# Kernel tuning notes

Measured on AMD Instinct MI355X. Metric: run time of the kernel, lower is better.

## Reference

```python
import jax, jax.numpy as jnp
import numpy as np

L, I, H = 4, 256, 512          # layers, input_size, hidden_size
SH, LH, GH = 4, 2, 2            # short/long/global heads
NH, HD, FF = SH + LH + GH, H // (SH + LH + GH), 2 * H
S, B = 1024, 8                  # seq (AST nodes), batch
EPS = 1e-5
NEG = -1e9


def _ln(x, g, b):
    m = jnp.mean(x, axis=-1, keepdims=True)
    v = jnp.var(x, axis=-1, keepdims=True)
    return (x - m) * jax.lax.rsqrt(v + EPS) * g + b


def setup_inputs() -> dict:
    key = jax.random.key(0)
    ks = jax.random.split(key, 10)
    w = lambda k, shape: jax.random.normal(k, shape, jnp.float32) * 0.02
    return {
        "nodes": jax.random.normal(ks[0], (S, B, I), jnp.float32),
        "dist": jax.random.randint(ks[1], (B, S, S), 0, 5, jnp.int32),
        "dense_w": w(ks[2], (H, I)), "dense_b": jnp.zeros((H,), jnp.float32),
        "dense_ln_g": jnp.ones((H,), jnp.float32), "dense_ln_b": jnp.zeros((H,), jnp.float32),
        "qkv_w": w(ks[3], (L, 3 * H, H)), "qkv_b": jnp.zeros((L, 3 * H), jnp.float32),
        "out_w": w(ks[4], (L, H, H)), "out_b": jnp.zeros((L, H), jnp.float32),
        "ln1_g": jnp.ones((L, H), jnp.float32), "ln1_b": jnp.zeros((L, H), jnp.float32),
        "ffn_w1": w(ks[5], (L, FF, H)), "ffn_b1": jnp.zeros((L, FF), jnp.float32),
        "ffn_w2": w(ks[6], (L, H, FF)), "ffn_b2": jnp.zeros((L, H), jnp.float32),
        "ln2_g": jnp.ones((L, H), jnp.float32), "ln2_b": jnp.zeros((L, H), jnp.float32),
        "bn_g": jnp.ones((H,), jnp.float32), "bn_b": jnp.zeros((H,), jnp.float32),
    }


def _mask_bias(dist):
    # dist: [B,S,S] int -> additive bias [B,NH,S,S]
    short = (dist == 1)[:, None]                       # [B,1,S,S]
    longm = (dist >= 1)[:, None]
    globm = jnp.broadcast_to((dist[:, 0:1, :] >= 1)[:, None], (dist.shape[0], 1, S, S))
    allowed = jnp.concatenate([
        jnp.broadcast_to(short, (dist.shape[0], SH, S, S)),
        jnp.broadcast_to(longm, (dist.shape[0], LH, S, S)),
        jnp.broadcast_to(globm, (dist.shape[0], GH, S, S)),
    ], axis=1)
    allowed = allowed | jnp.eye(S, dtype=bool)
    return jnp.where(allowed, 0.0, NEG).astype(jnp.float32)


def _forward(nodes, dist, dense_w, dense_b, dense_ln_g, dense_ln_b,
             qkv_w, qkv_b, out_w, out_b, ln1_g, ln1_b,
             ffn_w1, ffn_b1, ffn_w2, ffn_b2, ln2_g, ln2_b, bn_g, bn_b):
    x = jnp.transpose(nodes, (1, 0, 2))                # [B,S,I]
    x = _ln(x @ dense_w.T + dense_b, dense_ln_g, dense_ln_b)  # [B,S,H]
    bias = _mask_bias(dist)                            # [B,NH,S,S]
    scale = 1.0 / np.sqrt(HD)

    def layer(x, p):
        (wqkv, bqkv, wo, bo, g1, b1, w1, bf1, w2, bf2, g2, b2) = p
        qkv = x @ wqkv.T + bqkv                        # [B,S,3H]
        q, k, v = jnp.split(qkv, 3, axis=-1)
        q = q.reshape(B, S, NH, HD).transpose(0, 2, 1, 3)
        k = k.reshape(B, S, NH, HD).transpose(0, 2, 1, 3)
        v = v.reshape(B, S, NH, HD).transpose(0, 2, 1, 3)
        scores = jnp.einsum('bhqd,bhkd->bhqk', q, k) * scale + bias
        attn = jax.nn.softmax(scores, axis=-1)
        o = jnp.einsum('bhqk,bhkd->bhqd', attn, v)
        o = o.transpose(0, 2, 1, 3).reshape(B, S, H) @ wo.T + bo
        x = _ln(x + o, g1, b1)
        f = jax.nn.relu(x @ w1.T + bf1) @ w2.T + bf2
        x = _ln(x + f, g2, b2)
        return x, None

    params = (qkv_w, qkv_b, out_w, out_b, ln1_g, ln1_b,
              ffn_w1, ffn_b1, ffn_w2, ffn_b2, ln2_g, ln2_b)
    x, _ = jax.lax.scan(layer, x, params)
    hidden = x[:, 0]                                   # first token -> [B,H]
    m = jnp.mean(hidden, axis=0)
    v = jnp.var(hidden, axis=0)
    return (hidden - m) * jax.lax.rsqrt(v + EPS) * bn_g + bn_b


def reference(nodes, dist, dense_w, dense_b, dense_ln_g, dense_ln_b,
              qkv_w, qkv_b, out_w, out_b, ln1_g, ln1_b,
              ffn_w1, ffn_b1, ffn_w2, ffn_b2, ln2_g, ln2_b, bn_g, bn_b):
    return _forward(nodes, dist, dense_w, dense_b, dense_ln_g, dense_ln_b,
                    qkv_w, qkv_b, out_w, out_b, ln1_g, ln1_b,
                    ffn_w1, ffn_b1, ffn_w2, ffn_b2, ln2_g, ln2_b, bn_g, bn_b)
```

## Files before the change

### kernel.cpp

```cpp
#include <hip/hip_runtime.h>
#include <hip/hip_bf16.h>
#include <math.h>

#define LAYERS 4
#define IDIM 256
#define HDIM 512
#define NH 8
#define HD 64
#define FF 1024
#define SEQ 1024
#define BATCH 8
#define EPS 1e-5f

typedef __attribute__((ext_vector_type(8))) short short8;
typedef __attribute__((ext_vector_type(4))) short short4v;
typedef __attribute__((ext_vector_type(4))) float f32x4;
typedef __attribute__((ext_vector_type(4))) int int4v;
typedef __attribute__((ext_vector_type(2))) unsigned int uint2v;
typedef unsigned long long u64;

__device__ __forceinline__ short f2bf(float f) {
    unsigned u = __float_as_uint(f);
    u = (u + 0x7FFFu + ((u >> 16) & 1u)) >> 16;
    return (short)u;
}
__device__ __forceinline__ float bf2f(short s) {
    return __uint_as_float(((unsigned)(unsigned short)s) << 16);
}
__device__ __forceinline__ void gll16(const void* g, void* l) {
    __builtin_amdgcn_global_load_lds(
        (const __attribute__((address_space(1))) unsigned int*)g,
        (__attribute__((address_space(3))) unsigned int*)l, 16, 0, 0);
}

#define CVT_P0 131072u
#define CVT_P1 3276800u
#define CVT_P2 4325376u
#define CVT_P3 6422528u
#define CVT_TOT 8519680u
__global__ __launch_bounds__(256) void cvt_all(const float* __restrict__ s0, short* __restrict__ d0,
                                               const float* __restrict__ s1, short* __restrict__ d1,
                                               const float* __restrict__ s2, short* __restrict__ d2,
                                               const float* __restrict__ s3, short* __restrict__ d3,
                                               const float* __restrict__ s4, short* __restrict__ d4) {
    size_t i = ((size_t)blockIdx.x * 256 + threadIdx.x) * 4;
    const float* s; short* d; size_t off;
    if (i < CVT_P0)      { s = s0; d = d0; off = i; }
    else if (i < CVT_P1) { s = s1; d = d1; off = i - CVT_P0; }
    else if (i < CVT_P2) { s = s2; d = d2; off = i - CVT_P1; }
    else if (i < CVT_P3) { s = s3; d = d3; off = i - CVT_P2; }
    else                 { s = s4; d = d4; off = i - CVT_P3; }
    f32x4 f = *(const f32x4*)(s + off);
    short4v o = {f2bf(f[0]), f2bf(f[1]), f2bf(f[2]), f2bf(f[3])};
    *(short4v*)(d + off) = o;
}

__global__ __launch_bounds__(256) void transpose_nodes(const float* __restrict__ nodes,
                                                       short* __restrict__ xt) {
    size_t idx = ((size_t)blockIdx.x * 256 + threadIdx.x) * 4;
    int i  = idx & (IDIM - 1);
    int sb = idx >> 8;
    int b  = sb & (BATCH - 1);
    int s  = sb >> 3;
    f32x4 f = *(const f32x4*)(nodes + idx);
    short4v o = {f2bf(f[0]), f2bf(f[1]), f2bf(f[2]), f2bf(f[3])};
    *(short4v*)(xt + ((size_t)b * SEQ + s) * IDIM + i) = o;
}

__global__ __launch_bounds__(256) void build_masks(const int* __restrict__ dist,
                                                   u64* __restrict__ mS,
                                                   u64* __restrict__ mL,
                                                   u64* __restrict__ mG) {
    int t = blockIdx.x * 256 + threadIdx.x;
    int w = t & 15, q = (t >> 4) & 1023, b = t >> 14;
    const int4v* dp = (const int4v*)(dist + ((size_t)b * SEQ + q) * SEQ + w * 64);
    u64 bs = 0, bl = 0;
#pragma unroll
    for (int i = 0; i < 16; i++) {
        int4v d = dp[i];
#pragma unroll
        for (int j = 0; j < 4; j++) {
            bs |= (u64)(d[j] == 1) << (i * 4 + j);
            bl |= (u64)(d[j] >= 1) << (i * 4 + j);
        }
    }
    mS[((size_t)b * SEQ + q) * 16 + w] = bs;
    mL[((size_t)b * SEQ + q) * 16 + w] = bl;
    if (q == 0) mG[b * 16 + w] = bl;
}

template<int BM>
__global__ __launch_bounds__(256, 2)
void gemm_bf16(const short* __restrict__ A, const short* __restrict__ W,
               const float* __restrict__ bias, short* __restrict__ C,
               short* __restrict__ vt, int M, int N, int K, int relu) {
    __shared__ __align__(16) short As[BM * 64];
    __shared__ __align__(16) short Ws[128 * 64];
    const int tid = threadIdx.x;
    const int w = tid >> 6, lane = tid & 63;
    const int l15 = lane & 15, quad = lane >> 4;
    const int m0 = blockIdx.y * BM, n0 = blockIdx.x * 128;

    constexpr int NI = (BM == 128) ? 4 : 2;
    const int wm = (BM == 128) ? (w >> 1) * 64 : 0;
    const int wn = (BM == 128) ? (w & 1) * 64 : w * 32;

    f32x4 acc[4][NI];
#pragma unroll
    for (int mi = 0; mi < 4; mi++)
#pragma unroll
        for (int ni = 0; ni < NI; ni++) acc[mi][ni] = (f32x4){0.f, 0.f, 0.f, 0.f};

    const int r_in = lane >> 3;
    const int c8   = lane & 7;

    for (int k0 = 0; k0 < K; k0 += 64) {
#pragma unroll
        for (int rep = 0; rep < BM * 8 / 256; rep++) {
            int chunk = rep * 4 + w;
            int row = chunk * 8 + r_in;
            const short* src = A + (size_t)(m0 + row) * K + k0 + ((c8 ^ (row & 7)) << 3);
            gll16(src, (char*)As + chunk * 1024);
        }
#pragma unroll
        for (int rep = 0; rep < 4; rep++) {
            int chunk = rep * 4 + w;
            int row = chunk * 8 + r_in;
            const short* src = W + (size_t)(n0 + row) * K + k0 + ((c8 ^ (row & 7)) << 3);
            gll16(src, (char*)Ws + chunk * 1024);
        }
        __syncthreads();
#pragma unroll
        for (int ks = 0; ks < 2; ks++) {
            short8 af[4], wf[NI];
            const int dblk = ks * 4 + quad;
#pragma unroll
            for (int mi = 0; mi < 4; mi++) {
                int row = wm + mi * 16 + l15;
                af[mi] = *(const short8*)((const char*)As + row * 128 + ((dblk ^ (row & 7)) << 4));
            }
#pragma unroll
            for (int ni = 0; ni < NI; ni++) {
                int row = wn + ni * 16 + l15;
                wf[ni] = *(const short8*)((const char*)Ws + row * 128 + ((dblk ^ (row & 7)) << 4));
            }
#pragma unroll
            for (int mi = 0; mi < 4; mi++)
#pragma unroll
                for (int ni = 0; ni < NI; ni++)
                    acc[mi][ni] = __builtin_amdgcn_mfma_f32_16x16x32_bf16(
                        af[mi], wf[ni], acc[mi][ni], 0, 0, 0);
        }
        __syncthreads();
    }
    if (vt && n0 >= 1024) {
#pragma unroll
        for (int ni = 0; ni < NI; ni++) {
            int n = n0 + wn + ni * 16 + l15;
            int d = n - 1024, h = d >> 6, dd = d & 63;
            float bz = bias[n];
#pragma unroll
            for (int mi = 0; mi < 4; mi++) {
                int mbase = m0 + wm + mi * 16 + quad * 4;
                int b = mbase >> 10, s = mbase & 1023;
                int tile = s >> 6, j = (s & 63) >> 2;
                size_t off = ((size_t)(b * NH + h) * HD + dd) * SEQ
                           + tile * 64 + (j & 7) * 8 + (j >> 3) * 4;
                short4v pk;
#pragma unroll
                for (int r = 0; r < 4; r++) pk[r] = f2bf(acc[mi][ni][r] + bz);
                *(short4v*)(vt + off) = pk;
            }
        }
    } else {
#pragma unroll
        for (int ni = 0; ni < NI; ni++) {
            int n = n0 + wn + ni * 16 + l15;
            float bz = bias[n];
#pragma unroll
            for (int mi = 0; mi < 4; mi++) {
#pragma unroll
                for (int r = 0; r < 4; r++) {
                    int m = m0 + wm + mi * 16 + quad * 4 + r;
                    float v = acc[mi][ni][r] + bz;
                    if (relu) v = fmaxf(v, 0.f);
                    C[(size_t)m * N + n] = f2bf(v);
                }
            }
        }
    }
}

#define EXP2SC 0.18033688011112042f
__global__ __launch_bounds__(256, 4)
void attn_mfma(const short* __restrict__ qkv, const short* __restrict__ vt,
               const u64* __restrict__ maskS, const u64* __restrict__ maskL,
               const u64* __restrict__ maskG, short* __restrict__ out) {
    const int tid = threadIdx.x;
    const int w = tid >> 6, lane = tid & 63, l15 = lane & 15, quad = lane >> 4;
    const int p = blockIdx.x;
    const int g_ = (p & 7) + 8 * (p >> 7);
    const int qt = (p >> 3) & 15;
    const int b = g_ >> 3, h = g_ & 7;
    const int q = qt * 64 + w * 16 + l15;

    __shared__ __align__(16) short Ks[64 * 64];
    __shared__ __align__(16) short Vs[64 * 64];

    short8 qf[2];
    {
        const short* qrow = qkv + ((size_t)(b * SEQ + q) * 1536) + h * 64;
#pragma unroll
        for (int ks = 0; ks < 2; ks++)
            qf[ks] = *(const short8*)(qrow + ks * 32 + quad * 8);
    }
    const u64* mrow = (h < 4) ? (maskS + ((size_t)b * SEQ + q) * 16)
                   : (h < 6) ? (maskL + ((size_t)b * SEQ + q) * 16)
                   :           (maskG + (size_t)b * 16);

    f32x4 of[4];
#pragma unroll
    for (int mt = 0; mt < 4; mt++) of[mt] = (f32x4){0.f, 0.f, 0.f, 0.f};
    float lsum = 0.f;

    const int r_in = lane >> 3, c8 = lane & 7;
    for (int kt = 0; kt < SEQ; kt += 64) {
#pragma unroll
        for (int rep = 0; rep < 2; rep++) {
            int chunk = rep * 4 + w;
            int row = chunk * 8 + r_in;
            const short* ksrc = qkv + ((size_t)(b * SEQ + kt + row) * 1536) + 512 + h * 64 + ((c8 ^ (row & 7)) << 3);
            gll16(ksrc, (char*)Ks + chunk * 1024);
            const short* vsrc = vt + ((size_t)((b * NH + h) * HD + row) * SEQ) + kt + ((c8 ^ (row & 7)) << 3);
            gll16(vsrc, (char*)Vs + chunk * 1024);
        }
        __syncthreads();

        f32x4 sa[4];
#pragma unroll
        for (int g = 0; g < 4; g++) sa[g] = (f32x4){0.f, 0.f, 0.f, 0.f};
#pragma unroll
        for (int ks = 0; ks < 2; ks++) {
            const int dblk = ks * 4 + quad;
#pragma unroll
            for (int g = 0; g < 4; g++) {
                int row = g * 16 + l15;
                short8 kf = *(const short8*)((const char*)Ks + row * 128 + ((dblk ^ (row & 7)) << 4));
                sa[g] = __builtin_amdgcn_mfma_f32_16x16x32_bf16(kf, qf[ks], sa[g], 0, 0, 0);
            }
        }
        u64 mw = mrow[kt >> 6];
        if ((q >> 6) == (kt >> 6)) mw |= 1ull << (q & 63);
        short4v pfrag[4];
#pragma unroll
        for (int g = 0; g < 4; g++) {
            float pv[4];
#pragma unroll
            for (int r = 0; r < 4; r++) {
                int key = g * 16 + quad * 4 + r;
                float bias = ((mw >> key) & 1ull) ? 0.f : -1e9f;
                pv[r] = exp2f(fmaf(sa[g][r], EXP2SC, bias));
                lsum += pv[r];
            }
            uint2v pk;
            pk[0] = __builtin_amdgcn_perm(__float_as_uint(pv[1]), __float_as_uint(pv[0]), 0x07060302u);
            pk[1] = __builtin_amdgcn_perm(__float_as_uint(pv[3]), __float_as_uint(pv[2]), 0x07060302u);
            pfrag[g] = __builtin_bit_cast(short4v, pk);
        }
#pragma unroll
        for (int g01 = 0; g01 < 2; g01++) {
            const int u = g01 * 4 + quad;
#pragma unroll
            for (int mt = 0; mt < 4; mt++) {
                int row = mt * 16 + l15;
                short8 vv = *(const short8*)((const char*)Vs + row * 128 + ((u ^ (row & 7)) << 4));
                short4v vlo = {vv[0], vv[1], vv[2], vv[3]};
                short4v vhi = {vv[4], vv[5], vv[6], vv[7]};
                of[mt] = __builtin_amdgcn_mfma_f32_16x16x16bf16_1k(vlo, pfrag[g01], of[mt], 0, 0, 0);
                of[mt] = __builtin_amdgcn_mfma_f32_16x16x16bf16_1k(vhi, pfrag[g01 + 2], of[mt], 0, 0, 0);
            }
        }
        __syncthreads();
    }
    lsum += __shfl_xor(lsum, 16);
    lsum += __shfl_xor(lsum, 32);
    float inv = 1.f / lsum;
#pragma unroll
    for (int mt = 0; mt < 4; mt++) {
        short4v pk;
#pragma unroll
        for (int r = 0; r < 4; r++) pk[r] = f2bf(of[mt][r] * inv);
        *(short4v*)(out + ((size_t)(b * SEQ + q) * HDIM) + h * 64 + mt * 16 + quad * 4) = pk;
    }
}

__global__ __launch_bounds__(256) void ln_bf16(const short* __restrict__ x,
                                               const short* __restrict__ r,
                                               const float* __restrict__ g,
                                               const float* __restrict__ b,
                                               short* __restrict__ y) {
    const int wv = threadIdx.x >> 6, lane = threadIdx.x & 63;
    const size_t row = (size_t)blockIdx.x * 4 + wv;
    const size_t base = row * HDIM + lane * 8;
    short8 xv = *(const short8*)(x + base);
    float v[8];
#pragma unroll
    for (int i = 0; i < 8; i++) v[i] = bf2f(xv[i]);
    if (r) {
        short8 rv = *(const short8*)(r + base);
#pragma unroll
        for (int i = 0; i < 8; i++) v[i] += bf2f(rv[i]);
    }
    float s = 0.f, ss = 0.f;
#pragma unroll
    for (int i = 0; i < 8; i++) { s += v[i]; ss += v[i] * v[i]; }
#pragma unroll
    for (int off = 1; off < 64; off <<= 1) {
        s  += __shfl_xor(s, off);
        ss += __shfl_xor(ss, off);
    }
    const float mean = s * (1.f / HDIM);
    const float var  = ss * (1.f / HDIM) - mean * mean;
    const float inv  = rsqrtf(var + EPS);
    f32x4 g0 = *(const f32x4*)(g + lane * 8), g1 = *(const f32x4*)(g + lane * 8 + 4);
    f32x4 b0 = *(const f32x4*)(b + lane * 8), b1 = *(const f32x4*)(b + lane * 8 + 4);
    short8 o;
#pragma unroll
    for (int i = 0; i < 4; i++) o[i]     = f2bf((v[i]     - mean) * inv * g0[i] + b0[i]);
#pragma unroll
    for (int i = 0; i < 4; i++) o[i + 4] = f2bf((v[i + 4] - mean) * inv * g1[i] + b1[i]);
    *(short8*)(y + base) = o;
}

__global__ __launch_bounds__(256) void final_bn(const short* __restrict__ X,
                                                const float* __restrict__ g,
                                                const float* __restrict__ bb,
                                                float* __restrict__ out) {
    int h = blockIdx.x * 256 + threadIdx.x;
    if (h >= HDIM) return;
    float vals[BATCH];
    float m = 0.f;
#pragma unroll
    for (int b = 0; b < BATCH; b++) {
        vals[b] = bf2f(X[(size_t)b * SEQ * HDIM + h]);
        m += vals[b];
    }
    m *= (1.f / BATCH);
    float v = 0.f;
#pragma unroll
    for (int b = 0; b < BATCH; b++) { float d = vals[b] - m; v += d * d; }
    v *= (1.f / BATCH);
    float inv = rsqrtf(v + EPS);
#pragma unroll
    for (int b = 0; b < BATCH; b++)
        out[b * HDIM + h] = (vals[b] - m) * inv * g[h] + bb[h];
}

extern "C" void kernel_launch(void* const* d_in, const int* in_sizes, int n_in,
                              void* d_out, int out_size, void* d_ws, size_t ws_size,
                              hipStream_t stream) {
    const float* nodes      = (const float*)d_in[0];
    const int*   dist       = (const int*)  d_in[1];
    const float* dense_w    = (const float*)d_in[2];
    const float* dense_b    = (const float*)d_in[3];
    const float* dense_ln_g = (const float*)d_in[4];
    const float* dense_ln_b = (const float*)d_in[5];
    const float* qkv_w      = (const float*)d_in[6];
    const float* qkv_b      = (const float*)d_in[7];
    const float* out_w      = (const float*)d_in[8];
    const float* out_b      = (const float*)d_in[9];
    const float* ln1_g      = (const float*)d_in[10];
    const float* ln1_b      = (const float*)d_in[11];
    const float* ffn_w1     = (const float*)d_in[12];
    const float* ffn_b1     = (const float*)d_in[13];
    const float* ffn_w2     = (const float*)d_in[14];
    const float* ffn_b2     = (const float*)d_in[15];
    const float* ln2_g      = (const float*)d_in[16];
    const float* ln2_b      = (const float*)d_in[17];
    const float* bn_g       = (const float*)d_in[18];
    const float* bn_b       = (const float*)d_in[19];
    float* out = (float*)d_out;

    const int M = BATCH * SEQ;
    const size_t MB = 1024 * 1024;
    char* ws = (char*)d_ws;
    short* Wd   = (short*)(ws + 0 * MB);
    short* Wqkv = (short*)(ws + 1 * MB);
    short* Wo   = (short*)(ws + 9 * MB);
    short* W1   = (short*)(ws + 13 * MB);
    short* W2   = (short*)(ws + 18 * MB);
    u64*   mS   = (u64*)(ws + 23 * MB);
    u64*   mL   = (u64*)(ws + 24 * MB);
    u64*   mG   = (u64*)(ws + 25 * MB);
    short* X    = (short*)(ws + 26 * MB);
    short* QKV  = (short*)(ws + 34 * MB);
    short* Vt   = (short*)(ws + 58 * MB);
    short* AT   = (short*)(ws + 66 * MB);
    short* O2   = (short*)(ws + 74 * MB);
    short* XT   = QKV;
    short* F1   = QKV;
    short* F2   = AT;

    cvt_all<<<CVT_TOT / 1024, 256, 0, stream>>>(dense_w, Wd, qkv_w, Wqkv,
                                                out_w, Wo, ffn_w1, W1, ffn_w2, W2);
    transpose_nodes<<<(SEQ * BATCH * IDIM) / 1024, 256, 0, stream>>>(nodes, XT);
    build_masks<<<(BATCH * SEQ * 16) / 256, 256, 0, stream>>>(dist, mS, mL, mG);

    gemm_bf16<64><<<dim3(HDIM / 128, M / 64), 256, 0, stream>>>(
        XT, Wd, dense_b, O2, nullptr, M, HDIM, IDIM, 0);
    ln_bf16<<<M / 4, 256, 0, stream>>>(O2, nullptr, dense_ln_g, dense_ln_b, X);

    for (int l = 0; l < LAYERS; l++) {
        const short* wqkv = Wqkv + (size_t)l * 3 * HDIM * HDIM;
        const float* bqkv = qkv_b + (size_t)l * 3 * HDIM;
        const short* wo   = Wo + (size_t)l * HDIM * HDIM;
        const float* bo   = out_b + (size_t)l * HDIM;
        const short* w1   = W1 + (size_t)l * FF * HDIM;
        const float* b1   = ffn_b1 + (size_t)l * FF;
        const short* w2   = W2 + (size_t)l * HDIM * FF;
        const float* b2   = ffn_b2 + (size_t)l * HDIM;

        gemm_bf16<128><<<dim3(3 * HDIM / 128, M / 128), 256, 0, stream>>>(
            X, wqkv, bqkv, QKV, Vt, M, 3 * HDIM, HDIM, 0);
        attn_mfma<<<1024, 256, 0, stream>>>(QKV, Vt, mS, mL, mG, AT);
        gemm_bf16<64><<<dim3(HDIM / 128, M / 64), 256, 0, stream>>>(
            AT, wo, bo, O2, nullptr, M, HDIM, HDIM, 0);
        ln_bf16<<<M / 4, 256, 0, stream>>>(X, O2, ln1_g + l * HDIM, ln1_b + l * HDIM, X);
        gemm_bf16<128><<<dim3(FF / 128, M / 128), 256, 0, stream>>>(
            X, w1, b1, F1, nullptr, M, FF, HDIM, 1);
        gemm_bf16<64><<<dim3(HDIM / 128, M / 64), 256, 0, stream>>>(
            F1, w2, b2, F2, nullptr, M, HDIM, FF, 0);
        ln_bf16<<<M / 4, 256, 0, stream>>>(X, F2, ln2_g + l * HDIM, ln2_b + l * HDIM, X);
    }
    final_bn<<<(HDIM + 255) / 256, 256, 0, stream>>>(X, bn_g, bn_b, out);
}
```

Baseline: 645.0 us.

## Split attention over two key halves and merge partials in a reduce kernel

The attention kernel now splits each query tile's key range into two halves, doubling the grid to 2048 blocks. Each block writes a bf16 output normalised by its own partial softmax sum, plus that row sum, into a float buffer. A new reduce kernel then merges the two halves using weights derived from those row sums. The mask-bit extraction is also simplified to use a pre-shifted 32-bit word per group. The aim is more parallelism and shorter per-block serial loops, at the cost of an extra kernel launch per layer, extra global traffic for the partials, and some bf16 rounding of intermediate results.

```diff
diff --git a/kernel.cpp b/kernel.cpp
--- a/kernel.cpp
+++ b/kernel.cpp
@@ -195,12 +195,14 @@
 __global__ __launch_bounds__(256, 4)
 void attn_mfma(const short* __restrict__ qkv, const short* __restrict__ vt,
                const u64* __restrict__ maskS, const u64* __restrict__ maskL,
-               const u64* __restrict__ maskG, short* __restrict__ out) {
+               const u64* __restrict__ maskG,
+               short* __restrict__ opart, float* __restrict__ lpart) {
     const int tid = threadIdx.x;
     const int w = tid >> 6, lane = tid & 63, l15 = lane & 15, quad = lane >> 4;
     const int p = blockIdx.x;
-    const int g_ = (p & 7) + 8 * (p >> 7);
+    const int g_ = (p & 7) + 8 * (p >> 8);
     const int qt = (p >> 3) & 15;
+    const int split = (p >> 7) & 1;
     const int b = g_ >> 3, h = g_ & 7;
     const int q = qt * 64 + w * 16 + l15;
 
@@ -224,7 +226,8 @@
     float lsum = 0.f;
 
     const int r_in = lane >> 3, c8 = lane & 7;
-    for (int kt = 0; kt < SEQ; kt += 64) {
+    const int kt0 = split * 512;
+    for (int kt = kt0; kt < kt0 + 512; kt += 64) {
 #pragma unroll
         for (int rep = 0; rep < 2; rep++) {
             int chunk = rep * 4 + w;
@@ -251,14 +254,16 @@
         }
         u64 mw = mrow[kt >> 6];
         if ((q >> 6) == (kt >> 6)) mw |= 1ull << (q & 63);
+        u64 mq = mw >> (quad * 4);
+        unsigned mlo = (unsigned)mq, mhi = (unsigned)(mq >> 32);
         short4v pfrag[4];
 #pragma unroll
         for (int g = 0; g < 4; g++) {
+            unsigned mg = ((g & 2) ? mhi : mlo) >> ((g & 1) * 16);
             float pv[4];
 #pragma unroll
             for (int r = 0; r < 4; r++) {
-                int key = g * 16 + quad * 4 + r;
-                float bias = ((mw >> key) & 1ull) ? 0.f : -1e9f;
+                float bias = ((mg >> r) & 1u) ? 0.f : -1e9f;
                 pv[r] = exp2f(fmaf(sa[g][r], EXP2SC, bias));
                 lsum += pv[r];
             }
@@ -284,14 +289,35 @@
     }
     lsum += __shfl_xor(lsum, 16);
     lsum += __shfl_xor(lsum, 32);
-    float inv = 1.f / lsum;
+    float inv = (lsum > 0.f) ? 1.f / lsum : 0.f;
+    short* op = opart + (size_t)split * (BATCH * SEQ * HDIM);
 #pragma unroll
     for (int mt = 0; mt < 4; mt++) {
         short4v pk;
 #pragma unroll
         for (int r = 0; r < 4; r++) pk[r] = f2bf(of[mt][r] * inv);
-        *(short4v*)(out + ((size_t)(b * SEQ + q) * HDIM) + h * 64 + mt * 16 + quad * 4) = pk;
-    }
+        *(short4v*)(op + ((size_t)(b * SEQ + q) * HDIM) + h * 64 + mt * 16 + quad * 4) = pk;
+    }
+    if (quad == 0)
+        lpart[((size_t)(b * NH + h) * 2 + split) * SEQ + q] = lsum;
+}
+
+__global__ __launch_bounds__(256) void reduce_attn(short* __restrict__ opart,
+                                                   const float* __restrict__ lpart) {
+    size_t i = ((size_t)blockIdx.x * 256 + threadIdx.x) * 8;
+    int b = (int)(i >> 19);
+    int s = (int)(i >> 9) & 1023;
+    int h = ((int)i & 511) >> 6;
+    float l0 = lpart[((size_t)(b * NH + h) * 2 + 0) * SEQ + s];
+    float l1 = lpart[((size_t)(b * NH + h) * 2 + 1) * SEQ + s];
+    float winv = 1.f / (l0 + l1);
+    float w0 = l0 * winv, w1 = l1 * winv;
+    short8 a = *(const short8*)(opart + i);
+    short8 c = *(const short8*)(opart + i + (size_t)(BATCH * SEQ * HDIM));
+    short8 o;
+#pragma unroll
+    for (int k = 0; k < 8; k++) o[k] = f2bf(w0 * bf2f(a[k]) + w1 * bf2f(c[k]));
+    *(short8*)(opart + i) = o;
 }
 
 __global__ __launch_bounds__(256) void ln_bf16(const short* __restrict__ x,
@@ -384,22 +410,23 @@
     const int M = BATCH * SEQ;
     const size_t MB = 1024 * 1024;
     char* ws = (char*)d_ws;
-    short* Wd   = (short*)(ws + 0 * MB);
-    short* Wqkv = (short*)(ws + 1 * MB);
-    short* Wo   = (short*)(ws + 9 * MB);
-    short* W1   = (short*)(ws + 13 * MB);
-    short* W2   = (short*)(ws + 18 * MB);
-    u64*   mS   = (u64*)(ws + 23 * MB);
-    u64*   mL   = (u64*)(ws + 24 * MB);
-    u64*   mG   = (u64*)(ws + 25 * MB);
-    short* X    = (short*)(ws + 26 * MB);
-    short* QKV  = (short*)(ws + 34 * MB);
-    short* Vt   = (short*)(ws + 58 * MB);
-    short* AT   = (short*)(ws + 66 * MB);
-    short* O2   = (short*)(ws + 74 * MB);
-    short* XT   = QKV;
-    short* F1   = QKV;
-    short* F2   = AT;
+    short* Wd    = (short*)(ws + 0 * MB);
+    short* Wqkv  = (short*)(ws + 1 * MB);
+    short* Wo    = (short*)(ws + 9 * MB);
+    short* W1    = (short*)(ws + 13 * MB);
+    short* W2    = (short*)(ws + 18 * MB);
+    u64*   mS    = (u64*)(ws + 23 * MB);
+    u64*   mL    = (u64*)(ws + 24 * MB);
+    u64*   mG    = (u64*)(ws + 25 * MB);
+    float* Lpart = (float*)(ws + 25 * MB + 65536);
+    short* X     = (short*)(ws + 26 * MB);
+    short* QKV   = (short*)(ws + 34 * MB);
+    short* Vt    = (short*)(ws + 58 * MB);
+    short* AT    = (short*)(ws + 66 * MB);
+    short* O2    = (short*)(ws + 74 * MB);
+    short* XT    = QKV;
+    short* F1    = QKV;
+    short* F2    = AT;
 
     cvt_all<<<CVT_TOT / 1024, 256, 0, stream>>>(dense_w, Wd, qkv_w, Wqkv,
                                                 out_w, Wo, ffn_w1, W1, ffn_w2, W2);
@@ -422,7 +449,8 @@
 
         gemm_bf16<128><<<dim3(3 * HDIM / 128, M / 128), 256, 0, stream>>>(
             X, wqkv, bqkv, QKV, Vt, M, 3 * HDIM, HDIM, 0);
-        attn_mfma<<<1024, 256, 0, stream>>>(QKV, Vt, mS, mL, mG, AT);
+        attn_mfma<<<2048, 256, 0, stream>>>(QKV, Vt, mS, mL, mG, AT, Lpart);
+        reduce_attn<<<(M * HDIM) / (8 * 256), 256, 0, stream>>>(AT, Lpart);
         gemm_bf16<64><<<dim3(HDIM / 128, M / 64), 256, 0, stream>>>(
             AT, wo, bo, O2, nullptr, M, HDIM, HDIM, 0);
         ln_bf16<<<M / 4, 256, 0, stream>>>(X, O2, ln1_g + l * HDIM, ln1_b + l * HDIM, X);
```

Measured after the change: 667.5 us. 3.5% more time.
